# Kernel tuning notes

Measured on AMD Instinct MI355X. Metric: run time of the kernel, lower is better.

The kernel has to match this reference:

```python
import jax, jax.numpy as jnp
import numpy as np

N_V = 100000
N_E = 20000
NNZ = 1600000
D = 128


def setup_inputs() -> dict:
    key = jax.random.key(0)
    k1, k2, k3, k4, k5 = jax.random.split(key, 5)
    X = jax.random.normal(k1, (N_V, D), dtype=jnp.float32)
    W = jax.random.normal(k2, (D, D), dtype=jnp.float32) * (1.0 / np.sqrt(D))
    b = jax.random.normal(k3, (D,), dtype=jnp.float32) * 0.01
    v2e_src = jax.random.randint(k4, (NNZ,), 0, N_V, dtype=jnp.int32)
    v2e_dst = jax.random.randint(k5, (NNZ,), 0, N_E, dtype=jnp.int32)
    return {"X": X, "W": W, "b": b, "v2e_src": v2e_src, "v2e_dst": v2e_dst, "num_e": N_E}


def reference(X, W, b, v2e_src, v2e_dst, num_e):
    num_v = X.shape[0]
    ones = jnp.ones(v2e_src.shape[0], dtype=X.dtype)
    # node degrees (values of D_v diagonal) and hyperedge incidence counts
    deg_v = jax.ops.segment_sum(ones, v2e_src, num_segments=num_v)
    cnt_e = jax.ops.segment_sum(ones, v2e_dst, num_segments=num_e)

    # theta: linear layer
    Xt = X @ W.T + b  # [N_V, D]

    # v2e mean aggregation: per hyperedge, mean of incident vertex features
    Ysum = jax.ops.segment_sum(Xt[v2e_src], v2e_dst, num_segments=num_e)  # [N_E, D]
    Y = Ysum / jnp.maximum(cnt_e, 1.0)[:, None]

    # edge norm: torch scatter_reduce(reduce='mean', include_self=True) -> sum/(count+1)
    De_sum = jax.ops.segment_sum(deg_v[v2e_src], v2e_dst, num_segments=num_e)
    De = De_sum / (cnt_e + 1.0)
    De = jnp.where(De > 0, jax.lax.rsqrt(jnp.maximum(De, 1e-30)), 1.0)  # inf -> 1
    Y = De[:, None] * Y

    # e2v sum aggregation
    Xo = jax.ops.segment_sum(Y[v2e_dst], v2e_src, num_segments=num_v)  # [N_V, D]

    # D_v^{-1/2} sparse diagonal mm (zero-degree nodes -> 0)
    dvn = jnp.where(deg_v > 0, jax.lax.rsqrt(jnp.maximum(deg_v, 1e-30)), 0.0)
    Xo = dvn[:, None] * Xo

    # is_last=False: ReLU then dropout (dropout is identity in eval)
    return jax.nn.relu(Xo)
```

## Files before the change

### kernel.cpp

```cpp
#include <hip/hip_runtime.h>
#include <hip/hip_bf16.h>

#define NV 100000
#define NE 20000
#define DD 128
#define ESHIFT 7
#define VSHIFT 9
#define NBE 157
#define NBV 196
#define NBK 256
#define CHUNK 8192
#define PTHREADS 512
#define CAPE 11264
#define CAPV 9216

using bf16 = __hip_bfloat16;

typedef __attribute__((ext_vector_type(8))) short frag_ab;
typedef __attribute__((ext_vector_type(4))) float frag_cd;

__device__ __forceinline__ float uas(unsigned u) { union { unsigned u; float f; } c; c.u = u; return c.f; }
__device__ __forceinline__ unsigned pk2(float lo, float hi) {
    bf16 l = __float2bfloat16(lo), h = __float2bfloat16(hi);
    return (unsigned)(*(unsigned short*)&l) | ((unsigned)(*(unsigned short*)&h) << 16);
}
__device__ __forceinline__ void accum8(float* a, uint4 x) {
    a[0] += uas(x.x << 16); a[1] += uas(x.x & 0xffff0000u);
    a[2] += uas(x.y << 16); a[3] += uas(x.y & 0xffff0000u);
    a[4] += uas(x.z << 16); a[5] += uas(x.z & 0xffff0000u);
    a[6] += uas(x.w << 16); a[7] += uas(x.w & 0xffff0000u);
}
__device__ __forceinline__ int wave_incl_scan(int v, int lane) {
#pragma unroll
    for (int o = 1; o < 64; o <<= 1) {
        int x = __shfl_up(v, o);
        if (lane >= o) v += x;
    }
    return v;
}

__global__ __launch_bounds__(PTHREADS) void partition_and_cvt(const int* __restrict__ src, const int* __restrict__ dst,
                                                              int* __restrict__ bcur_e, int* __restrict__ bcur_v,
                                                              unsigned* __restrict__ pairs_e, unsigned* __restrict__ pairs_v,
                                                              int nnz,
                                                              const float4* __restrict__ Xf, ushort4* __restrict__ Xb,
                                                              const float4* __restrict__ Wf, ushort4* __restrict__ Wb) {
    int nchunk = (nnz + CHUNK - 1) / CHUNK;
    int t = threadIdx.x;
    int bid = blockIdx.x;
    if (bid >= 2 * nchunk) {
        const int n4x = NV * DD / 4;
        const int n4w = DD * DD / 4;
        int i = (bid - 2 * nchunk) * PTHREADS + t;
        if (i < n4x + n4w) {
            float4 v;
            ushort4 o;
            if (i < n4x) v = Xf[i]; else v = Wf[i - n4x];
            bf16 a = __float2bfloat16(v.x); o.x = *(unsigned short*)&a;
            bf16 b = __float2bfloat16(v.y); o.y = *(unsigned short*)&b;
            bf16 c = __float2bfloat16(v.z); o.z = *(unsigned short*)&c;
            bf16 d = __float2bfloat16(v.w); o.w = *(unsigned short*)&d;
            if (i < n4x) Xb[i] = o; else Wb[i - n4x] = o;
        }
        return;
    }
    __shared__ int cntA[NBK], cntB[NBK], pre1[NBK], loff[NBK], gbase[NBK], wsum[4];
    __shared__ int totValid;
    __shared__ unsigned stage[CHUNK];
    int phase = (bid >= nchunk) ? 1 : 0;
    int cidx = phase ? bid - nchunk : bid;
    int sub = t >> 8;
    int lane = t & 63;
    int base = cidx * CHUNK;
    unsigned p[16];
    int rk[16];
#pragma unroll
    for (int k = 0; k < 16; ++k) {
        int i = base + k * PTHREADS + t;
        p[k] = (i < nnz) ? (((unsigned)src[i] << 15) | (unsigned)dst[i]) : 0xFFFFFFFFu;
    }

    if (t < NBK) { cntA[t] = 0; cntB[t] = 0; }
    __syncthreads();
#pragma unroll
    for (int k = 0; k < 16; ++k)
        if (p[k] != 0xFFFFFFFFu) {
            int b = phase ? (int)(p[k] >> 24) : (int)((p[k] >> ESHIFT) & 0xFF);
            rk[k] = atomicAdd(sub ? &cntB[b] : &cntA[b], 1);
        }
    __syncthreads();
    {
        int incl = 0, tv = 0;
        if (t < NBK) {
            int a = cntA[t], bb = cntB[t];
            tv = a + bb;
            pre1[t] = a;
            incl = wave_incl_scan(tv, lane);
            if (lane == 63) wsum[t >> 6] = incl;
        }
        __syncthreads();
        if (t == 0) { int r = 0; for (int i = 0; i < 4; ++i) { int x = wsum[i]; wsum[i] = r; r += x; } }
        __syncthreads();
        if (t < NBK) {
            int ex = incl - tv + wsum[t >> 6];
            loff[t] = ex;
            int rel = (tv > 0) ? atomicAdd(phase ? &bcur_v[t] : &bcur_e[t], tv) : 0;
            gbase[t] = t * (phase ? CAPV : CAPE) + rel;
            if (t == NBK - 1) totValid = ex + tv;
        }
    }
    __syncthreads();
#pragma unroll
    for (int k = 0; k < 16; ++k)
        if (p[k] != 0xFFFFFFFFu) {
            int b = phase ? (int)(p[k] >> 24) : (int)((p[k] >> ESHIFT) & 0xFF);
            stage[loff[b] + rk[k] + (sub ? pre1[b] : 0)] = p[k];
        }
    __syncthreads();
    unsigned* outp = phase ? pairs_v : pairs_e;
    for (int i = t; i < totValid; i += PTHREADS) {
        unsigned pp = stage[i];
        int b = phase ? (int)(pp >> 24) : (int)((pp >> ESHIFT) & 0xFF);
        outp[gbase[b] + i - loff[b]] = pp;
    }
}

__global__ __launch_bounds__(1024) void build_csr(const unsigned* __restrict__ pairs_e, const int* __restrict__ bcur_e,
                                                  int* __restrict__ off_e, int* __restrict__ end_e, int* __restrict__ e_src,
                                                  const unsigned* __restrict__ pairs_v, const int* __restrict__ bcur_v,
                                                  int* __restrict__ off_v, unsigned short* __restrict__ v_edge,
                                                  int* __restrict__ deg_v) {
    __shared__ int cA[2048], cB[2048], sc2[512], eoff[512], wsumS[8];
    int t = threadIdx.x;
    cA[t] = 0; cA[t + 1024] = 0;
    __syncthreads();
    if ((int)blockIdx.x < NBE) {
        int b = blockIdx.x;
        int lo = b * CAPE, hi = lo + bcur_e[b];
        int sub = t >> 7;
        unsigned pv[12];
        int rk[12];
        int kk = 0;
        for (int i = lo + t; i < hi; i += 1024, ++kk) {
            unsigned p = pairs_e[i];
            pv[kk] = p;
            rk[kk] = atomicAdd(&cA[sub * 128 + (p & 127)], 1);
        }
        __syncthreads();
        if (t < 128) {
            int run = 0;
#pragma unroll
            for (int s = 0; s < 8; ++s) { cB[s * 128 + t] = run; run += cA[s * 128 + t]; }
            sc2[t] = run;
        }
        __syncthreads();
        int incl = 0, myrun = 0;
        if (t < 128) {
            myrun = sc2[t];
            incl = wave_incl_scan(myrun, t & 63);
            if ((t & 63) == 63) wsumS[t >> 6] = incl;
        }
        __syncthreads();
        if (t == 0) { int r = 0; for (int i = 0; i < 2; ++i) { int x = wsumS[i]; wsumS[i] = r; r += x; } }
        __syncthreads();
        if (t < 128) {
            int ex = incl - myrun + wsumS[t >> 6];
            eoff[t] = ex;
            int e = (b << ESHIFT) + t;
            if (e < NE) { off_e[e] = lo + ex; end_e[e] = lo + ex + myrun; }
        }
        __syncthreads();
        for (int k = 0; k < kk; ++k) {
            int bkt = pv[k] & 127;
            int pos = lo + eoff[bkt] + cB[sub * 128 + bkt] + rk[k];
            e_src[pos] = (int)(pv[k] >> 15);
        }
    } else {
        int b = blockIdx.x - NBE;
        int lo = b * CAPV, hi = lo + bcur_v[b];
        int sub = t >> 8;
        unsigned pv[9];
        int rk[9];
        int kk = 0;
        for (int i = lo + t; i < hi; i += 1024, ++kk) {
            unsigned p = pairs_v[i];
            pv[kk] = p;
            rk[kk] = atomicAdd(&cA[sub * 512 + ((p >> 15) & 511)], 1);
        }
        __syncthreads();
        if (t < 512) {
            int run = 0;
#pragma unroll
            for (int s = 0; s < 4; ++s) { cB[s * 512 + t] = run; run += cA[s * 512 + t]; }
            sc2[t] = run;
        }
        __syncthreads();
        int incl = 0, myrun = 0;
        if (t < 512) {
            myrun = sc2[t];
            incl = wave_incl_scan(myrun, t & 63);
            if ((t & 63) == 63) wsumS[t >> 6] = incl;
        }
        __syncthreads();
        if (t == 0) { int r = 0; for (int i = 0; i < 8; ++i) { int x = wsumS[i]; wsumS[i] = r; r += x; } }
        __syncthreads();
        if (t < 512) {
            int ex = incl - myrun + wsumS[t >> 6];
            eoff[t] = ex;
            int v = (b << VSHIFT) + t;
            if (v < NV) { off_v[v] = lo + ex; deg_v[v] = myrun; }
        }
        __syncthreads();
        for (int k = 0; k < kk; ++k) {
            int bkt = (pv[k] >> 15) & 511;
            int pos = lo + eoff[bkt] + cB[sub * 512 + bkt] + rk[k];
            v_edge[pos] = (unsigned short)(pv[k] & 0x7FFF);
        }
    }
}

__global__ __launch_bounds__(512) void edge_fused(const uint4* __restrict__ Xq, const int* __restrict__ off_e,
                                                  const int* __restrict__ end_e,
                                                  const int* __restrict__ e_src, const int* __restrict__ deg_v,
                                                  const bf16* __restrict__ Wb, const float* __restrict__ bias,
                                                  bf16* __restrict__ Y) {
    __shared__ short Stile[16][136];
    __shared__ float betaL[16];
    int t = threadIdx.x;
    int w = t >> 6, lane = t & 63;
    int h = lane >> 5;
    int g2 = (lane >> 4) & 1;
    int l16 = lane & 15;
    int mBase = blockIdx.x * 16;
    int le = w * 2 + g2;
    int e = mBase + le;
    int start = off_e[e], end = end_e[e];
    int cnt = end - start;
    int half0 = (cnt + 1) >> 1;
    int hs = start + h * half0;
    int he = h ? end : (start + half0);
    float acc[8] = {0.f, 0.f, 0.f, 0.f, 0.f, 0.f, 0.f, 0.f};
    float degsum = 0.f;
    int j = hs;
    for (; j + 8 <= he; j += 8) {
        int s0 = e_src[j + 0], s1 = e_src[j + 1], s2 = e_src[j + 2], s3 = e_src[j + 3];
        int s4 = e_src[j + 4], s5 = e_src[j + 5], s6 = e_src[j + 6], s7 = e_src[j + 7];
        uint4 x0 = Xq[(size_t)s0 * 16 + l16];
        uint4 x1 = Xq[(size_t)s1 * 16 + l16];
        uint4 x2 = Xq[(size_t)s2 * 16 + l16];
        uint4 x3 = Xq[(size_t)s3 * 16 + l16];
        uint4 x4 = Xq[(size_t)s4 * 16 + l16];
        uint4 x5 = Xq[(size_t)s5 * 16 + l16];
        uint4 x6 = Xq[(size_t)s6 * 16 + l16];
        uint4 x7 = Xq[(size_t)s7 * 16 + l16];
        degsum += (float)(deg_v[s0] + deg_v[s1] + deg_v[s2] + deg_v[s3]
                        + deg_v[s4] + deg_v[s5] + deg_v[s6] + deg_v[s7]);
        accum8(acc, x0); accum8(acc, x1); accum8(acc, x2); accum8(acc, x3);
        accum8(acc, x4); accum8(acc, x5); accum8(acc, x6); accum8(acc, x7);
    }
    for (; j + 4 <= he; j += 4) {
        int s0 = e_src[j + 0], s1 = e_src[j + 1], s2 = e_src[j + 2], s3 = e_src[j + 3];
        uint4 x0 = Xq[(size_t)s0 * 16 + l16];
        uint4 x1 = Xq[(size_t)s1 * 16 + l16];
        uint4 x2 = Xq[(size_t)s2 * 16 + l16];
        uint4 x3 = Xq[(size_t)s3 * 16 + l16];
        degsum += (float)(deg_v[s0] + deg_v[s1] + deg_v[s2] + deg_v[s3]);
        accum8(acc, x0); accum8(acc, x1); accum8(acc, x2); accum8(acc, x3);
    }
    for (; j < he; ++j) {
        int s = e_src[j];
        uint4 x = Xq[(size_t)s * 16 + l16];
        degsum += (float)deg_v[s];
        accum8(acc, x);
    }
#pragma unroll
    for (int r = 0; r < 8; ++r) acc[r] += __shfl_xor(acc[r], 32);
    degsum += __shfl_xor(degsum, 32);

    float cntf = (float)cnt;
    float Des = degsum / (cntf + 1.0f);
    float De = (Des > 0.f) ? rsqrtf(fmaxf(Des, 1e-30f)) : 1.0f;
    float scale = De / fmaxf(cntf, 1.0f);
    if (h == 0) {
        uint4 o;
        o.x = pk2(acc[0] * scale, acc[1] * scale);
        o.y = pk2(acc[2] * scale, acc[3] * scale);
        o.z = pk2(acc[4] * scale, acc[5] * scale);
        o.w = pk2(acc[6] * scale, acc[7] * scale);
        *(uint4*)&Stile[le][l16 * 8] = o;
        if (l16 == 0) betaL[le] = (cntf > 0.f) ? De : 0.f;
    }
    __syncthreads();

    const short* Ws = (const short*)Wb;
    int quad = lane >> 4;
    frag_ab a[4];
#pragma unroll
    for (int kt = 0; kt < 4; ++kt)
        a[kt] = *(const frag_ab*)&Stile[l16][kt * 32 + quad * 8];
    float beta_r[4];
#pragma unroll
    for (int r = 0; r < 4; ++r) beta_r[r] = betaL[quad * 4 + r];

    int nt = w;
    frag_cd acc2 = {0.f, 0.f, 0.f, 0.f};
#pragma unroll
    for (int kt = 0; kt < 4; ++kt) {
        frag_ab bfr = *(const frag_ab*)(Ws + (size_t)(nt * 16 + l16) * DD + kt * 32 + quad * 8);
        acc2 = __builtin_amdgcn_mfma_f32_16x16x32_bf16(a[kt], bfr, acc2, 0, 0, 0);
    }
    float bv = bias[nt * 16 + l16];
#pragma unroll
    for (int r = 0; r < 4; ++r) {
        int row = mBase + quad * 4 + r;
        float v = acc2[r] + beta_r[r] * bv;
        Y[(size_t)row * DD + nt * 16 + l16] = __float2bfloat16(v);
    }
}

__global__ __launch_bounds__(256) void vertex_agg(const uint4* __restrict__ Yq, const int* __restrict__ off_v,
                                                  const int* __restrict__ deg_v,
                                                  const unsigned short* __restrict__ v_edge, float* __restrict__ out) {
    int wave = (blockIdx.x * blockDim.x + threadIdx.x) >> 6;
    int lane = threadIdx.x & 63;
    int g = lane >> 4, l16 = lane & 15;
    int v = wave * 4 + g;
    if (v >= NV) return;
    int start = off_v[v], deg = deg_v[v];
    int end = start + deg;
    float acc[8] = {0.f, 0.f, 0.f, 0.f, 0.f, 0.f, 0.f, 0.f};
    int j = start;
    for (; j + 8 <= end; j += 8) {
        int e0 = v_edge[j + 0], e1 = v_edge[j + 1], e2 = v_edge[j + 2], e3 = v_edge[j + 3];
        int e4 = v_edge[j + 4], e5 = v_edge[j + 5], e6 = v_edge[j + 6], e7 = v_edge[j + 7];
        uint4 y0 = Yq[(size_t)e0 * 16 + l16];
        uint4 y1 = Yq[(size_t)e1 * 16 + l16];
        uint4 y2 = Yq[(size_t)e2 * 16 + l16];
        uint4 y3 = Yq[(size_t)e3 * 16 + l16];
        uint4 y4 = Yq[(size_t)e4 * 16 + l16];
        uint4 y5 = Yq[(size_t)e5 * 16 + l16];
        uint4 y6 = Yq[(size_t)e6 * 16 + l16];
        uint4 y7 = Yq[(size_t)e7 * 16 + l16];
        accum8(acc, y0); accum8(acc, y1); accum8(acc, y2); accum8(acc, y3);
        accum8(acc, y4); accum8(acc, y5); accum8(acc, y6); accum8(acc, y7);
    }
    for (; j + 4 <= end; j += 4) {
        int e0 = v_edge[j + 0], e1 = v_edge[j + 1], e2 = v_edge[j + 2], e3 = v_edge[j + 3];
        uint4 y0 = Yq[(size_t)e0 * 16 + l16];
        uint4 y1 = Yq[(size_t)e1 * 16 + l16];
        uint4 y2 = Yq[(size_t)e2 * 16 + l16];
        uint4 y3 = Yq[(size_t)e3 * 16 + l16];
        accum8(acc, y0); accum8(acc, y1); accum8(acc, y2); accum8(acc, y3);
    }
    for (; j < end; ++j) {
        int e = v_edge[j];
        uint4 y = Yq[(size_t)e * 16 + l16];
        accum8(acc, y);
    }
    float dvn = (deg > 0) ? rsqrtf((float)deg) : 0.f;
    float4 o1, o2;
    o1.x = fmaxf(acc[0] * dvn, 0.f);
    o1.y = fmaxf(acc[1] * dvn, 0.f);
    o1.z = fmaxf(acc[2] * dvn, 0.f);
    o1.w = fmaxf(acc[3] * dvn, 0.f);
    o2.x = fmaxf(acc[4] * dvn, 0.f);
    o2.y = fmaxf(acc[5] * dvn, 0.f);
    o2.z = fmaxf(acc[6] * dvn, 0.f);
    o2.w = fmaxf(acc[7] * dvn, 0.f);
    float4* op = (float4*)(out + (size_t)v * DD + l16 * 8);
    op[0] = o1;
    op[1] = o2;
}

extern "C" void kernel_launch(void* const* d_in, const int* in_sizes, int n_in,
                              void* d_out, int out_size, void* d_ws, size_t ws_size,
                              hipStream_t stream) {
    const float* X = (const float*)d_in[0];
    const float* W = (const float*)d_in[1];
    const float* b = (const float*)d_in[2];
    const int* src = (const int*)d_in[3];
    const int* dst = (const int*)d_in[4];
    int nnz = in_sizes[3];

    char* ws = (char*)d_ws;
    size_t o = 0;
    auto take = [&](size_t bytes) -> char* {
        char* p = ws + o;
        o += (bytes + 255) & ~(size_t)255;
        return p;
    };
    int* bcur_e = (int*)take((size_t)2 * NBK * 4);
    int* bcur_v = bcur_e + NBK;
    int* off_e = (int*)take((size_t)NE * 4);
    int* end_e = (int*)take((size_t)NE * 4);
    int* off_v = (int*)take((size_t)NV * 4);
    int* deg_v = (int*)take((size_t)NV * 4);
    int* e_src = (int*)take((size_t)NBE * CAPE * 4);
    unsigned short* v_edge = (unsigned short*)take((size_t)NBV * CAPV * 2);
    unsigned* pairs_e = (unsigned*)take((size_t)NBE * CAPE * 4);
    unsigned* pairs_v = (unsigned*)take((size_t)NBV * CAPV * 4);
    bf16* Y = (bf16*)take((size_t)NE * DD * 2);
    bf16* Wb = (bf16*)take((size_t)DD * DD * 2);
    bf16* Xb = (bf16*)take((size_t)NV * DD * 2);
    (void)ws_size; (void)n_in; (void)out_size;

    int nchunk = (nnz + CHUNK - 1) / CHUNK;
    int ncvt = (NV * DD / 4 + DD * DD / 4 + PTHREADS - 1) / PTHREADS;

    hipMemsetAsync(bcur_e, 0, (size_t)2 * NBK * 4, stream);
    partition_and_cvt<<<2 * nchunk + ncvt, PTHREADS, 0, stream>>>(src, dst, bcur_e, bcur_v, pairs_e, pairs_v, nnz,
                                                                  (const float4*)X, (ushort4*)Xb,
                                                                  (const float4*)W, (ushort4*)Wb);
    build_csr<<<NBE + NBV, 1024, 0, stream>>>(pairs_e, bcur_e, off_e, end_e, e_src,
                                              pairs_v, bcur_v, off_v, v_edge, deg_v);
    edge_fused<<<NE / 16, 512, 0, stream>>>((const uint4*)Xb, off_e, end_e, e_src, deg_v, Wb, b, Y);
    vertex_agg<<<(NV / 4 * 64) / 256, 256, 0, stream>>>((const uint4*)Y, off_v, deg_v, v_edge, (float*)d_out);
}
```

Before: 241.4 us.

## Move vertex CSR build into edge kernel and compute degrees via global atomics

Splits the combined CSR build so only the edge CSR runs before the edge aggregation kernel. The vertex-side bucket sort now runs as extra blocks of the edge kernel, overlapping with edge aggregation. Vertex degrees are counted with global atomics during partitioning, since the edge kernel needs deg_v before the vertex CSR exists. This adds 1.6M global atomics and a two-pass reread of pairs_v in exchange for removing a serial dependency.

Result: slower. 296.8 us (+22.9%).

```diff
diff --git a/kernel.cpp b/kernel.cpp
--- a/kernel.cpp
+++ b/kernel.cpp
@@ -42,7 +42,7 @@
 __global__ __launch_bounds__(PTHREADS) void partition_and_cvt(const int* __restrict__ src, const int* __restrict__ dst,
                                                               int* __restrict__ bcur_e, int* __restrict__ bcur_v,
                                                               unsigned* __restrict__ pairs_e, unsigned* __restrict__ pairs_v,
-                                                              int nnz,
+                                                              int* __restrict__ deg_v, int nnz,
                                                               const float4* __restrict__ Xf, ushort4* __restrict__ Xb,
                                                               const float4* __restrict__ Wf, ushort4* __restrict__ Wb) {
     int nchunk = (nnz + CHUNK - 1) / CHUNK;
@@ -87,6 +87,7 @@
         if (p[k] != 0xFFFFFFFFu) {
             int b = phase ? (int)(p[k] >> 24) : (int)((p[k] >> ESHIFT) & 0xFF);
             rk[k] = atomicAdd(sub ? &cntB[b] : &cntA[b], 1);
+            if (!phase) atomicAdd(&deg_v[p[k] >> 15], 1);
         }
     __syncthreads();
     {
@@ -125,113 +126,107 @@
     }
 }
 
-__global__ __launch_bounds__(1024) void build_csr(const unsigned* __restrict__ pairs_e, const int* __restrict__ bcur_e,
-                                                  int* __restrict__ off_e, int* __restrict__ end_e, int* __restrict__ e_src,
-                                                  const unsigned* __restrict__ pairs_v, const int* __restrict__ bcur_v,
-                                                  int* __restrict__ off_v, unsigned short* __restrict__ v_edge,
-                                                  int* __restrict__ deg_v) {
-    __shared__ int cA[2048], cB[2048], sc2[512], eoff[512], wsumS[8];
+__global__ __launch_bounds__(1024) void csr_e(const unsigned* __restrict__ pairs_e, const int* __restrict__ bcur_e,
+                                              int* __restrict__ off_e, int* __restrict__ end_e, int* __restrict__ e_src) {
+    __shared__ int cA[1024], cB[1024], sc2[128], eoff[128], wsumS[2];
     int t = threadIdx.x;
-    cA[t] = 0; cA[t + 1024] = 0;
-    __syncthreads();
-    if ((int)blockIdx.x < NBE) {
-        int b = blockIdx.x;
-        int lo = b * CAPE, hi = lo + bcur_e[b];
-        int sub = t >> 7;
-        unsigned pv[12];
-        int rk[12];
-        int kk = 0;
-        for (int i = lo + t; i < hi; i += 1024, ++kk) {
-            unsigned p = pairs_e[i];
-            pv[kk] = p;
-            rk[kk] = atomicAdd(&cA[sub * 128 + (p & 127)], 1);
-        }
-        __syncthreads();
-        if (t < 128) {
-            int run = 0;
-#pragma unroll
-            for (int s = 0; s < 8; ++s) { cB[s * 128 + t] = run; run += cA[s * 128 + t]; }
-            sc2[t] = run;
-        }
-        __syncthreads();
-        int incl = 0, myrun = 0;
-        if (t < 128) {
-            myrun = sc2[t];
-            incl = wave_incl_scan(myrun, t & 63);
-            if ((t & 63) == 63) wsumS[t >> 6] = incl;
-        }
-        __syncthreads();
-        if (t == 0) { int r = 0; for (int i = 0; i < 2; ++i) { int x = wsumS[i]; wsumS[i] = r; r += x; } }
-        __syncthreads();
-        if (t < 128) {
-            int ex = incl - myrun + wsumS[t >> 6];
-            eoff[t] = ex;
-            int e = (b << ESHIFT) + t;
-            if (e < NE) { off_e[e] = lo + ex; end_e[e] = lo + ex + myrun; }
-        }
-        __syncthreads();
-        for (int k = 0; k < kk; ++k) {
-            int bkt = pv[k] & 127;
-            int pos = lo + eoff[bkt] + cB[sub * 128 + bkt] + rk[k];
-            e_src[pos] = (int)(pv[k] >> 15);
-        }
-    } else {
-        int b = blockIdx.x - NBE;
-        int lo = b * CAPV, hi = lo + bcur_v[b];
-        int sub = t >> 8;
-        unsigned pv[9];
-        int rk[9];
-        int kk = 0;
-        for (int i = lo + t; i < hi; i += 1024, ++kk) {
-            unsigned p = pairs_v[i];
-            pv[kk] = p;
-            rk[kk] = atomicAdd(&cA[sub * 512 + ((p >> 15) & 511)], 1);
-        }
-        __syncthreads();
-        if (t < 512) {
-            int run = 0;
-#pragma unroll
-            for (int s = 0; s < 4; ++s) { cB[s * 512 + t] = run; run += cA[s * 512 + t]; }
-            sc2[t] = run;
-        }
-        __syncthreads();
-        int incl = 0, myrun = 0;
-        if (t < 512) {
-            myrun = sc2[t];
-            incl = wave_incl_scan(myrun, t & 63);
-            if ((t & 63) == 63) wsumS[t >> 6] = incl;
-        }
-        __syncthreads();
-        if (t == 0) { int r = 0; for (int i = 0; i < 8; ++i) { int x = wsumS[i]; wsumS[i] = r; r += x; } }
-        __syncthreads();
-        if (t < 512) {
-            int ex = incl - myrun + wsumS[t >> 6];
-            eoff[t] = ex;
-            int v = (b << VSHIFT) + t;
-            if (v < NV) { off_v[v] = lo + ex; deg_v[v] = myrun; }
-        }
-        __syncthreads();
-        for (int k = 0; k < kk; ++k) {
-            int bkt = (pv[k] >> 15) & 511;
-            int pos = lo + eoff[bkt] + cB[sub * 512 + bkt] + rk[k];
-            v_edge[pos] = (unsigned short)(pv[k] & 0x7FFF);
-        }
-    }
-}
-
-__global__ __launch_bounds__(512) void edge_fused(const uint4* __restrict__ Xq, const int* __restrict__ off_e,
+    cA[t] = 0;
+    __syncthreads();
+    int b = blockIdx.x;
+    int lo = b * CAPE, hi = lo + bcur_e[b];
+    int sub = t >> 7;
+    unsigned pv[12];
+    int rk[12];
+    int kk = 0;
+    for (int i = lo + t; i < hi; i += 1024, ++kk) {
+        unsigned p = pairs_e[i];
+        pv[kk] = p;
+        rk[kk] = atomicAdd(&cA[sub * 128 + (p & 127)], 1);
+    }
+    __syncthreads();
+    if (t < 128) {
+        int run = 0;
+#pragma unroll
+        for (int s = 0; s < 8; ++s) { cB[s * 128 + t] = run; run += cA[s * 128 + t]; }
+        sc2[t] = run;
+    }
+    __syncthreads();
+    int incl = 0, myrun = 0;
+    if (t < 128) {
+        myrun = sc2[t];
+        incl = wave_incl_scan(myrun, t & 63);
+        if ((t & 63) == 63) wsumS[t >> 6] = incl;
+    }
+    __syncthreads();
+    if (t == 0) { int r = 0; for (int i = 0; i < 2; ++i) { int x = wsumS[i]; wsumS[i] = r; r += x; } }
+    __syncthreads();
+    if (t < 128) {
+        int ex = incl - myrun + wsumS[t >> 6];
+        eoff[t] = ex;
+        int e = (b << ESHIFT) + t;
+        if (e < NE) { off_e[e] = lo + ex; end_e[e] = lo + ex + myrun; }
+    }
+    __syncthreads();
+    for (int k = 0; k < kk; ++k) {
+        int bkt = pv[k] & 127;
+        int pos = lo + eoff[bkt] + cB[sub * 128 + bkt] + rk[k];
+        e_src[pos] = (int)(pv[k] >> 15);
+    }
+}
+
+__global__ __launch_bounds__(512) void edge_vsort(const uint4* __restrict__ Xq, const int* __restrict__ off_e,
                                                   const int* __restrict__ end_e,
                                                   const int* __restrict__ e_src, const int* __restrict__ deg_v,
                                                   const bf16* __restrict__ Wb, const float* __restrict__ bias,
-                                                  bf16* __restrict__ Y) {
+                                                  bf16* __restrict__ Y,
+                                                  const unsigned* __restrict__ pairs_v, const int* __restrict__ bcur_v,
+                                                  int* __restrict__ off_v, unsigned short* __restrict__ v_edge) {
     __shared__ short Stile[16][136];
     __shared__ float betaL[16];
+    __shared__ int vA[1024], vB[512], veoff[512], vws[8];
     int t = threadIdx.x;
+    int bid = blockIdx.x;
+
+    if (bid < NBV) {
+        int b = bid;
+        int lo = b * CAPV, hi = lo + bcur_v[b];
+        int sub = t >> 8;
+        vA[t] = 0; vA[t + 512] = 0;
+        __syncthreads();
+        for (int i = lo + t; i < hi; i += 512)
+            atomicAdd(&vA[sub * 512 + ((pairs_v[i] >> 15) & 511)], 1);
+        __syncthreads();
+        int cnt0 = vA[t], cnt1 = vA[512 + t];
+        int myrun = cnt0 + cnt1;
+        int lane = t & 63;
+        int incl = wave_incl_scan(myrun, lane);
+        if (lane == 63) vws[t >> 6] = incl;
+        __syncthreads();
+        if (t == 0) { int r = 0; for (int i = 0; i < 8; ++i) { int x = vws[i]; vws[i] = r; r += x; } }
+        __syncthreads();
+        int ex = incl - myrun + vws[t >> 6];
+        veoff[t] = ex;
+        vB[t] = cnt0;
+        int v = (b << VSHIFT) + t;
+        if (v < NV) off_v[v] = lo + ex;
+        __syncthreads();
+        vA[t] = 0; vA[t + 512] = 0;
+        __syncthreads();
+        for (int i = lo + t; i < hi; i += 512) {
+            unsigned p = pairs_v[i];
+            int v9 = (p >> 15) & 511;
+            int r = atomicAdd(&vA[sub * 512 + v9], 1);
+            int pos = lo + veoff[v9] + (sub ? vB[v9] : 0) + r;
+            v_edge[pos] = (unsigned short)(p & 0x7FFF);
+        }
+        return;
+    }
+
     int w = t >> 6, lane = t & 63;
     int h = lane >> 5;
     int g2 = (lane >> 4) & 1;
     int l16 = lane & 15;
-    int mBase = blockIdx.x * 16;
+    int mBase = (bid - NBV) * 16;
     int le = w * 2 + g2;
     int e = mBase + le;
     int start = off_e[e], end = end_e[e];
@@ -389,12 +384,12 @@
         o += (bytes + 255) & ~(size_t)255;
         return p;
     };
-    int* bcur_e = (int*)take((size_t)2 * NBK * 4);
+    int* bcur_e = (int*)take((size_t)(2 * NBK + NV) * 4);
     int* bcur_v = bcur_e + NBK;
+    int* deg_v = bcur_e + 2 * NBK;
     int* off_e = (int*)take((size_t)NE * 4);
     int* end_e = (int*)take((size_t)NE * 4);
     int* off_v = (int*)take((size_t)NV * 4);
-    int* deg_v = (int*)take((size_t)NV * 4);
     int* e_src = (int*)take((size_t)NBE * CAPE * 4);
     unsigned short* v_edge = (unsigned short*)take((size_t)NBV * CAPV * 2);
     unsigned* pairs_e = (unsigned*)take((size_t)NBE * CAPE * 4);
@@ -407,12 +402,13 @@
     int nchunk = (nnz + CHUNK - 1) / CHUNK;
     int ncvt = (NV * DD / 4 + DD * DD / 4 + PTHREADS - 1) / PTHREADS;
 
-    hipMemsetAsync(bcur_e, 0, (size_t)2 * NBK * 4, stream);
-    partition_and_cvt<<<2 * nchunk + ncvt, PTHREADS, 0, stream>>>(src, dst, bcur_e, bcur_v, pairs_e, pairs_v, nnz,
+    hipMemsetAsync(bcur_e, 0, (size_t)(2 * NBK + NV) * 4, stream);
+    partition_and_cvt<<<2 * nchunk + ncvt, PTHREADS, 0, stream>>>(src, dst, bcur_e, bcur_v, pairs_e, pairs_v,
+                                                                  deg_v, nnz,
                                                                   (const float4*)X, (ushort4*)Xb,
                                                                   (const float4*)W, (ushort4*)Wb);
-    build_csr<<<NBE + NBV, 1024, 0, stream>>>(pairs_e, bcur_e, off_e, end_e, e_src,
-                                              pairs_v, bcur_v, off_v, v_edge, deg_v);
-    edge_fused<<<NE / 16, 512, 0, stream>>>((const uint4*)Xb, off_e, end_e, e_src, deg_v, Wb, b, Y);
+    csr_e<<<NBE, 1024, 0, stream>>>(pairs_e, bcur_e, off_e, end_e, e_src);
+    edge_vsort<<<NBV + NE / 16, 512, 0, stream>>>((const uint4*)Xb, off_e, end_e, e_src, deg_v, Wb, b, Y,
+                                                  pairs_v, bcur_v, off_v, v_edge);
     vertex_agg<<<(NV / 4 * 64) / 256, 256, 0, stream>>>((const uint4*)Y, off_v, deg_v, v_edge, (float*)d_out);
 }
```
